# Kernel optimization log

Hardware: AMD Instinct MI355X
Metric: run time of the kernel (lower is better)

The kernel has to match this reference:

```python
import jax, jax.numpy as jnp
import numpy as np

B, C, H, W = 16, 256, 32, 32
AD, SC, R = 16, 32, 4


def _conv1x1(x, w, b):
    # x: [B,Cin,H,W], w: [Cout,Cin], b: [Cout]
    return jnp.einsum('oc,bchw->bohw', w, x) + b[None, :, None, None]


def setup_inputs() -> dict:
    key = jax.random.key(0)
    ks = jax.random.split(key, 12)
    p = lambda k, shape: (jax.random.normal(k, shape, dtype=jnp.float32) * 0.02)
    return {
        'x': jax.random.normal(ks[0], (B, C, H, W), dtype=jnp.float32),
        'fc1_w': p(ks[1], (C // R, C)), 'fc1_b': jnp.zeros((C // R,), jnp.float32),
        'fc2_w': p(ks[2], (C, C // R)), 'fc2_b': jnp.zeros((C,), jnp.float32),
        'qkv_w': p(ks[3], (AD * 2 + SC, SC)), 'qkv_b': jnp.zeros((AD * 2 + SC,), jnp.float32),
        'proj_w': p(ks[4], (SC, SC)), 'proj_b': jnp.zeros((SC,), jnp.float32),
        'ffn1_w': p(ks[5], (4 * C, C)), 'ffn1_b': jnp.zeros((4 * C,), jnp.float32),
        'ffn2_w': p(ks[6], (C, 4 * C)), 'ffn2_b': jnp.zeros((C,), jnp.float32),
    }


def reference(x, fc1_w, fc1_b, fc2_w, fc2_b, qkv_w, qkv_b, proj_w, proj_b,
              ffn1_w, ffn1_b, ffn2_w, ffn2_b):
    # --- DynamicChannelSelect: SE gate then channel split ---
    s = x.mean(axis=(2, 3), keepdims=True)                       # [B,C,1,1]
    s = jax.nn.relu(_conv1x1(s, fc1_w, fc1_b))
    s = jax.nn.sigmoid(_conv1x1(s, fc2_w, fc2_b))
    xg = x * s
    attn_part, non_attn_part = xg[:, :SC], xg[:, SC:]

    # --- SHSA: single-head self-attention on SC channels ---
    qkv = _conv1x1(attn_part, qkv_w, qkv_b)                      # [B,2*AD+SC,H,W]
    q = qkv[:, :AD].reshape(B, AD, H * W)
    k = qkv[:, AD:2 * AD].reshape(B, AD, H * W)
    v = qkv[:, 2 * AD:].reshape(B, SC, H * W)
    scale = AD ** -0.5
    attn = jax.nn.softmax(jnp.einsum('bcn,bcm->bnm', q, k) * scale, axis=-1)  # [B,N,N]
    out = jnp.einsum('bcm,bnm->bcn', v, attn).reshape(B, SC, H, W)
    attn_out = _conv1x1(out, proj_w, proj_b)

    # --- concat + 1x1-conv FFN ---
    y = jnp.concatenate([attn_out, non_attn_part], axis=1)       # [B,C,H,W]
    h = jax.nn.relu(_conv1x1(y, ffn1_w, ffn1_b))                 # [B,4C,H,W]
    return _conv1x1(h, ffn2_w, ffn2_b)                           # [B,C,H,W]
```

## Files before the change

kernel.cpp:

```cpp
#include <hip/hip_runtime.h>
#include <cstdint>
#include <cstddef>

#define BB 16
#define CC 256
#define NP 1024

typedef __attribute__((ext_vector_type(8))) short bf16x8;
typedef __attribute__((ext_vector_type(4))) float f32x4;
typedef unsigned short u16;

__device__ __forceinline__ u16 f2bf(float f) {
    union { float f; uint32_t u; } v; v.f = f;
    uint32_t u = v.u;
    return (u16)((u + 0x7FFFu + ((u >> 16) & 1u)) >> 16);
}

__global__ __launch_bounds__(256)
void se_mean_conv_kernel(const float* __restrict__ x, float* __restrict__ s_mean,
                         const float* __restrict__ w1, u16* __restrict__ d1,
                         const float* __restrict__ w2, u16* __restrict__ d2) {
    int blk = blockIdx.x;
    int t = threadIdx.x;
    if (blk < BB * CC) {
        const float* p = x + (size_t)blk * NP;
        float4 v = *(const float4*)(p + t * 4);
        float s = (v.x + v.y) + (v.z + v.w);
#pragma unroll
        for (int off = 32; off; off >>= 1) s += __shfl_down(s, off, 64);
        __shared__ float red[4];
        if ((t & 63) == 0) red[t >> 6] = s;
        __syncthreads();
        if (t == 0) s_mean[blk] = (red[0] + red[1] + red[2] + red[3]) * (1.0f / NP);
    } else {
        int blk2 = blk - BB * CC;
        const float* src = (blk2 < 256) ? w1 : w2;
        u16* dst = (blk2 < 256) ? d1 : d2;
        int i = ((blk2 & 255) * 256 + t) * 4;
        float4 v = *(const float4*)(src + i);
        ushort4 o;
        o.x = f2bf(v.x); o.y = f2bf(v.y); o.z = f2bf(v.z); o.w = f2bf(v.w);
        *(ushort4*)(dst + i) = o;
    }
}

__global__ __launch_bounds__(256)
void se_mlp_kernel(const float* __restrict__ s_mean,
                   const float* __restrict__ fc1_w, const float* __restrict__ fc1_b,
                   const float* __restrict__ fc2_w, const float* __restrict__ fc2_b,
                   float* __restrict__ sig) {
    int b = blockIdx.x, t = threadIdx.x;
    __shared__ float sm[256];
    __shared__ float part[4][64];
    __shared__ float h1[64];
    sm[t] = s_mean[b * 256 + t];
    __syncthreads();
    int to = t & 63, g = t >> 6;
    float a = 0.f;
#pragma unroll 8
    for (int c = 0; c < 64; ++c) a += fc1_w[to * 256 + g * 64 + c] * sm[g * 64 + c];
    part[g][to] = a;
    __syncthreads();
    if (t < 64) h1[t] = fmaxf(part[0][t] + part[1][t] + part[2][t] + part[3][t] + fc1_b[t], 0.f);
    __syncthreads();
    float acc = fc2_b[t];
#pragma unroll 8
    for (int j = 0; j < 64; ++j) acc += fc2_w[t * 64 + j] * h1[j];
    sig[b * 256 + t] = 1.f / (1.f + __expf(-acc));
}

__global__ __launch_bounds__(256)
void scale_transpose_qkv_kernel(const float* __restrict__ x, const float* __restrict__ sig,
                                const float* __restrict__ qW, const float* __restrict__ qB,
                                u16* __restrict__ ygt, u16* __restrict__ Qt,
                                u16* __restrict__ Kt, u16* __restrict__ Vb) {
    int nt = blockIdx.x, ct = blockIdx.y, b = blockIdx.z;
    __shared__ float tile[64][65];
    __shared__ float ws[64 * 32];
    __shared__ float bs[64];
    __shared__ float vtile[32][64];
    __shared__ float sig_l[64];
    int t = threadIdx.x;
    const float* Xb = x + ((size_t)b * CC + ct * 64) * NP + nt * 64;
    if (t < 64) sig_l[t] = sig[b * 256 + ct * 64 + t];
    if (ct == 0) {
        for (int e = t; e < 2048; e += 256) ws[e] = qW[e];
        if (t < 64) bs[t] = qB[t];
    }
#pragma unroll
    for (int p = 0; p < 4; ++p) {
        int e = t + p * 256;
        int c = e >> 4, n4 = (e & 15) * 4;
        float4 v = *(const float4*)&Xb[(size_t)c * NP + n4];
        tile[c][n4] = v.x; tile[c][n4 + 1] = v.y; tile[c][n4 + 2] = v.z; tile[c][n4 + 3] = v.w;
    }
    __syncthreads();
    u16* Yb = ygt + ((size_t)b * NP + nt * 64) * CC + ct * 64;
#pragma unroll
    for (int p = 0; p < 4; ++p) {
        int e = t + p * 256;
        int n = e >> 4, c4 = (e & 15) * 4;
        if (ct * 64 + c4 >= 32) {
            ushort4 o;
            o.x = f2bf(tile[c4][n] * sig_l[c4]);
            o.y = f2bf(tile[c4 + 1][n] * sig_l[c4 + 1]);
            o.z = f2bf(tile[c4 + 2][n] * sig_l[c4 + 2]);
            o.w = f2bf(tile[c4 + 3][n] * sig_l[c4 + 3]);
            *(ushort4*)&Yb[(size_t)n * CC + c4] = o;
        }
    }
    if (ct == 0) {
        int nn = t & 63, g = t >> 6;
        int n = nt * 64 + nn;
        float xs[32];
#pragma unroll
        for (int c = 0; c < 32; ++c) xs[c] = tile[c][nn] * sig_l[c];
        float acc[16];
#pragma unroll
        for (int oc = 0; oc < 16; ++oc) {
            int o = g * 16 + oc;
            float a = bs[o];
#pragma unroll
            for (int c = 0; c < 32; ++c) a += ws[o * 32 + c] * xs[c];
            acc[oc] = a;
        }
        if (g == 0) {
            u16* qr = Qt + ((size_t)b * NP + n) * 32;
            ushort4 z4; z4.x = 0; z4.y = 0; z4.z = 0; z4.w = 0;
#pragma unroll
            for (int j = 0; j < 16; j += 4) {
                ushort4 o4;
                o4.x = f2bf(acc[j] * 0.25f);     o4.y = f2bf(acc[j + 1] * 0.25f);
                o4.z = f2bf(acc[j + 2] * 0.25f); o4.w = f2bf(acc[j + 3] * 0.25f);
                *(ushort4*)&qr[j] = o4;
            }
            *(ushort4*)&qr[16] = z4; *(ushort4*)&qr[20] = z4;
            *(ushort4*)&qr[24] = z4; *(ushort4*)&qr[28] = z4;
        } else if (g == 1) {
            u16* kr = Kt + ((size_t)b * NP + n) * 32;
            ushort4 z4; z4.x = 0; z4.y = 0; z4.z = 0; z4.w = 0;
#pragma unroll
            for (int j = 0; j < 16; j += 4) {
                ushort4 k4;
                k4.x = f2bf(acc[j]);     k4.y = f2bf(acc[j + 1]);
                k4.z = f2bf(acc[j + 2]); k4.w = f2bf(acc[j + 3]);
                *(ushort4*)&kr[j] = k4;
            }
            *(ushort4*)&kr[16] = z4; *(ushort4*)&kr[20] = z4;
            *(ushort4*)&kr[24] = z4; *(ushort4*)&kr[28] = z4;
        } else {
#pragma unroll
            for (int oc = 0; oc < 16; ++oc) vtile[(g - 2) * 16 + oc][nn] = acc[oc];
        }
        __syncthreads();
        for (int e = t; e < 2048; e += 256) {
            int c = e >> 6, nn2 = e & 63;
            Vb[(size_t)b * 32 * NP + (size_t)c * NP + nt * 64 + nn2] = f2bf(vtile[c][nn2]);
        }
    }
}

__global__ __launch_bounds__(256)
void attn_mfma_kernel(const u16* __restrict__ Qt, const u16* __restrict__ Kt,
                      const u16* __restrict__ Vb,
                      const float* __restrict__ proj_w, const float* __restrict__ proj_b,
                      u16* __restrict__ ygt) {
    int b = blockIdx.x & 15;
    int n0 = (blockIdx.x >> 4) * 16;
    __shared__ __align__(16) u16 P_lds[4][16][40];
    __shared__ float al_lds[4][16];
    __shared__ float sm_lds[4][16];
    __shared__ float sl_lds[4][16];
    __shared__ float O_lds[4][16][33];
    __shared__ float pw_s[32][32];
    __shared__ float pb_s[32];
    int t = threadIdx.x;
    int w = t >> 6, lane = t & 63;
    int q = lane >> 4, idx = lane & 15;

    for (int e = t; e < 1024; e += 256) pw_s[e >> 5][e & 31] = proj_w[e];
    if (t < 32) pb_s[t] = proj_b[t];
    __syncthreads();

    const u16* Qb = Qt + (size_t)b * NP * 32;
    const u16* Kb = Kt + (size_t)b * NP * 32;
    const u16* Vp = Vb + (size_t)b * 32 * NP;

    int nrow = n0 + idx;
    bf16x8 aq = *(const bf16x8*)&Qb[(size_t)nrow * 32 + q * 8];

    f32x4 O0 = {0.f, 0.f, 0.f, 0.f}, O1 = {0.f, 0.f, 0.f, 0.f};
    float m_run[4] = {-1e30f, -1e30f, -1e30f, -1e30f};
    float l_run[4] = {0.f, 0.f, 0.f, 0.f};

    int mbase = w * 256;
    for (int m0 = mbase; m0 < mbase + 256; m0 += 32) {
        bf16x8 bk0 = *(const bf16x8*)&Kb[(size_t)(m0 + idx) * 32 + q * 8];
        bf16x8 bk1 = *(const bf16x8*)&Kb[(size_t)(m0 + 16 + idx) * 32 + q * 8];
        bf16x8 va0 = *(const bf16x8*)&Vp[(size_t)idx * NP + m0 + q * 8];
        bf16x8 va1 = *(const bf16x8*)&Vp[(size_t)(16 + idx) * NP + m0 + q * 8];
        f32x4 z = {0.f, 0.f, 0.f, 0.f};
        f32x4 S0 = __builtin_amdgcn_mfma_f32_16x16x32_bf16(aq, bk0, z, 0, 0, 0);
        f32x4 S1 = __builtin_amdgcn_mfma_f32_16x16x32_bf16(aq, bk1, z, 0, 0, 0);
        float mx[4], p0[4], p1[4], alpha[4];
#pragma unroll
        for (int r = 0; r < 4; ++r) mx[r] = fmaxf(S0[r], S1[r]);
#pragma unroll
        for (int off = 1; off < 16; off <<= 1)
#pragma unroll
            for (int r = 0; r < 4; ++r) mx[r] = fmaxf(mx[r], __shfl_xor(mx[r], off, 64));
#pragma unroll
        for (int r = 0; r < 4; ++r) {
            float nm = fmaxf(m_run[r], mx[r]);
            alpha[r] = __expf(m_run[r] - nm);
            m_run[r] = nm;
            p0[r] = __expf(S0[r] - nm);
            p1[r] = __expf(S1[r] - nm);
        }
#pragma unroll
        for (int r = 0; r < 4; ++r) {
            float s = p0[r] + p1[r];
#pragma unroll
            for (int off = 1; off < 16; off <<= 1) s += __shfl_xor(s, off, 64);
            l_run[r] = l_run[r] * alpha[r] + s;
        }
#pragma unroll
        for (int r = 0; r < 4; ++r) {
            P_lds[w][q * 4 + r][idx]      = f2bf(p0[r]);
            P_lds[w][q * 4 + r][idx + 16] = f2bf(p1[r]);
        }
        if (idx == 0) {
#pragma unroll
            for (int r = 0; r < 4; ++r) al_lds[w][q * 4 + r] = alpha[r];
        }
        float an = al_lds[w][idx];
#pragma unroll
        for (int r = 0; r < 4; ++r) { O0[r] *= an; O1[r] *= an; }
        bf16x8 pf = *(const bf16x8*)&P_lds[w][idx][q * 8];
        O0 = __builtin_amdgcn_mfma_f32_16x16x32_bf16(va0, pf, O0, 0, 0, 0);
        O1 = __builtin_amdgcn_mfma_f32_16x16x32_bf16(va1, pf, O1, 0, 0, 0);
    }
    if (idx == 0) {
#pragma unroll
        for (int r = 0; r < 4; ++r) {
            sm_lds[w][q * 4 + r] = m_run[r];
            sl_lds[w][q * 4 + r] = l_run[r];
        }
    }
#pragma unroll
    for (int r = 0; r < 4; ++r) {
        O_lds[w][idx][q * 4 + r]      = O0[r];
        O_lds[w][idx][q * 4 + r + 16] = O1[r];
    }
    __syncthreads();
    if (w == 0) {
        float m0_ = sm_lds[0][idx], m1 = sm_lds[1][idx], m2 = sm_lds[2][idx], m3 = sm_lds[3][idx];
        float gm = fmaxf(fmaxf(m0_, m1), fmaxf(m2, m3));
        float e0 = __expf(m0_ - gm), e1 = __expf(m1 - gm);
        float e2 = __expf(m2 - gm), e3 = __expf(m3 - gm);
        float linv = 1.f / (sl_lds[0][idx] * e0 + sl_lds[1][idx] * e1 +
                            sl_lds[2][idx] * e2 + sl_lds[3][idx] * e3);
#pragma unroll
        for (int r = 0; r < 4; ++r) {
            int c0 = q * 4 + r;
            O_lds[0][idx][c0] = (O_lds[0][idx][c0] * e0 + O_lds[1][idx][c0] * e1 +
                                 O_lds[2][idx][c0] * e2 + O_lds[3][idx][c0] * e3) * linv;
            int c1 = c0 + 16;
            O_lds[0][idx][c1] = (O_lds[0][idx][c1] * e0 + O_lds[1][idx][c1] * e1 +
                                 O_lds[2][idx][c1] * e2 + O_lds[3][idx][c1] * e3) * linv;
        }
        float o0[4], o1[4];
#pragma unroll
        for (int r = 0; r < 4; ++r) { o0[r] = pb_s[q * 4 + r]; o1[r] = pb_s[q * 4 + r + 16]; }
#pragma unroll
        for (int c = 0; c < 32; ++c) {
            float xv = O_lds[0][idx][c];
#pragma unroll
            for (int r = 0; r < 4; ++r) {
                o0[r] += pw_s[q * 4 + r][c] * xv;
                o1[r] += pw_s[q * 4 + r + 16][c] * xv;
            }
        }
        u16* yrow = ygt + ((size_t)b * NP + n0 + idx) * CC;
        ushort4 w0, w1;
        w0.x = f2bf(o0[0]); w0.y = f2bf(o0[1]); w0.z = f2bf(o0[2]); w0.w = f2bf(o0[3]);
        w1.x = f2bf(o1[0]); w1.y = f2bf(o1[1]); w1.z = f2bf(o1[2]); w1.w = f2bf(o1[3]);
        *(ushort4*)&yrow[q * 4] = w0;
        *(ushort4*)&yrow[q * 4 + 16] = w1;
    }
}

__global__ __launch_bounds__(512, 2)
void ffn_fused_kernel(const u16* __restrict__ w1b, const u16* __restrict__ w2b,
                      const u16* __restrict__ ygt,
                      const float* __restrict__ bias1, const float* __restrict__ bias2,
                      float* __restrict__ out) {
    __shared__ __align__(16) u16 Ys[4][64][64];
    __shared__ __align__(16) u16 Hs[2][64][64];
    __shared__ __align__(16) u16 W2s[2][256][64];
    __shared__ float Bs1[1024];
    int t = threadIdx.x;
    int w = t >> 6, lane = t & 63;
    int q = lane >> 4, idx = lane & 15;
    int srow = lane >> 3;
    int gch = (lane & 7) ^ srow;
    int n0 = blockIdx.x * 64;
    int rot = blockIdx.x & 7;
    int hh = w >> 2, wm = w & 3;

#define ISSUE_W2S(sc_)                                                                     \
    {                                                                                      \
        _Pragma("unroll")                                                                  \
        for (int e = 0; e < 8; ++e) {                                                      \
            int hh2 = e >> 2, rnd = e & 3;                                                 \
            int rw = rnd * 64 + w * 8;                                                     \
            __builtin_amdgcn_global_load_lds(                                              \
                (const __attribute__((address_space(1))) void*)(w2b + (size_t)(rw + srow) * 1024 + (sc_) * 128 + hh2 * 64 + gch * 8), \
                (__attribute__((address_space(3))) void*)(&W2s[hh2][rw][0]),               \
                16, 0, 0);                                                                 \
        }                                                                                  \
    }

#define LOAD_AF(dst, sc_)                                                                  \
    {                                                                                      \
        const u16* a1 = w1b + ((size_t)((sc_) * 128 + w * 16 + idx)) * CC;                 \
        _Pragma("unroll")                                                                  \
        for (int s = 0; s < 8; ++s) dst[s] = *(const bf16x8*)(a1 + s * 32 + q * 8);        \
    }

#pragma unroll
    for (int e = 0; e < 4; ++e) {
        __builtin_amdgcn_global_load_lds(
            (const __attribute__((address_space(1))) void*)(ygt + (size_t)(n0 + w * 8 + srow) * CC + e * 64 + gch * 8),
            (__attribute__((address_space(3))) void*)(&Ys[e][w * 8][0]),
            16, 0, 0);
    }
    Bs1[t] = bias1[t];
    Bs1[t + 512] = bias1[t + 512];

    f32x4 oacc[4][4];
#pragma unroll
    for (int f = 0; f < 4; ++f)
#pragma unroll
        for (int j = 0; j < 4; ++j) { f32x4 z = {0.f, 0.f, 0.f, 0.f}; oacc[f][j] = z; }

    ISSUE_W2S(rot)
    bf16x8 af[8];
    LOAD_AF(af, rot)
    __syncthreads();

    for (int it = 0; it < 8; ++it) {
        int sc  = (it + rot) & 7;
        int scn = (it + 1 + rot) & 7;
        bf16x8 afn[8];
        if (it + 1 < 8) LOAD_AF(afn, scn)

        f32x4 hacc[4];
#pragma unroll
        for (int j = 0; j < 4; ++j) { f32x4 z = {0.f, 0.f, 0.f, 0.f}; hacc[j] = z; }
#pragma unroll
        for (int s = 0; s < 8; ++s) {
            int kb = s >> 1, h2 = s & 1;
#pragma unroll
            for (int j = 0; j < 4; ++j) {
                bf16x8 yb = *(const bf16x8*)&Ys[kb][j * 16 + idx][(((q + 4 * h2) ^ (idx & 7)) * 8)];
                hacc[j] = __builtin_amdgcn_mfma_f32_16x16x32_bf16(af[s], yb, hacc[j], 0, 0, 0);
            }
        }

        int mb = sc * 128 + w * 16 + q * 4;
        float b0 = Bs1[mb], b1v = Bs1[mb + 1], b2v = Bs1[mb + 2], b3v = Bs1[mb + 3];
        int chk_hi = wm * 2 + (q >> 1);
#pragma unroll
        for (int j = 0; j < 4; ++j) {
            int n = j * 16 + idx;
            int chk = chk_hi ^ (n & 7);
            uint32_t lo = (uint32_t)f2bf(fmaxf(hacc[j][0] + b0, 0.f)) |
                          ((uint32_t)f2bf(fmaxf(hacc[j][1] + b1v, 0.f)) << 16);
            uint32_t hi = (uint32_t)f2bf(fmaxf(hacc[j][2] + b2v, 0.f)) |
                          ((uint32_t)f2bf(fmaxf(hacc[j][3] + b3v, 0.f)) << 16);
            uint32_t* hp = (uint32_t*)&Hs[hh][n][chk * 8 + (q & 1) * 4];
            hp[0] = lo; hp[1] = hi;
        }
        __syncthreads();

#pragma unroll
        for (int s2 = 0; s2 < 2; ++s2) {
            bf16x8 a2f[4];
#pragma unroll
            for (int f = 0; f < 4; ++f)
                a2f[f] = *(const bf16x8*)&W2s[hh][wm * 64 + f * 16 + idx][(((q + 4 * s2) ^ (idx & 7)) * 8)];
#pragma unroll
            for (int j = 0; j < 4; ++j) {
                bf16x8 hb = *(const bf16x8*)&Hs[hh][j * 16 + idx][(((q + 4 * s2) ^ (idx & 7)) * 8)];
#pragma unroll
                for (int f = 0; f < 4; ++f)
                    oacc[f][j] = __builtin_amdgcn_mfma_f32_16x16x32_bf16(a2f[f], hb, oacc[f][j], 0, 0, 0);
            }
        }
        __syncthreads();

        if (it + 1 < 8) {
            ISSUE_W2S(scn)
#pragma unroll
            for (int s = 0; s < 8; ++s) af[s] = afn[s];
        }
    }
#undef ISSUE_W2S
#undef LOAD_AF

    float* R = (float*)&W2s[0][0][0];
    if (w >= 4) {
#pragma unroll
        for (int f = 0; f < 4; ++f)
#pragma unroll
            for (int j = 0; j < 4; ++j)
#pragma unroll
                for (int r = 0; r < 4; ++r)
                    R[(wm * 64 + f * 16 + q * 4 + r) * 64 + j * 16 + idx] = oacc[f][j][r];
    }
    __syncthreads();
    if (w < 4) {
        int b = n0 >> 10, nnb = n0 & 1023;
#pragma unroll
        for (int f = 0; f < 4; ++f) {
            int m2 = wm * 64 + f * 16 + q * 4;
            float c0 = bias2[m2], c1 = bias2[m2 + 1], c2 = bias2[m2 + 2], c3 = bias2[m2 + 3];
#pragma unroll
            for (int j = 0; j < 4; ++j) {
                int col = j * 16 + idx;
                const float* Rp = &R[m2 * 64 + col];
                float* p = out + ((size_t)b * CC + m2) * NP + nnb + col;
                f32x4 v = oacc[f][j];
                p[0]      = v.x + c0 + Rp[0];
                p[NP]     = v.y + c1 + Rp[64];
                p[2 * NP] = v.z + c2 + Rp[128];
                p[3 * NP] = v.w + c3 + Rp[192];
            }
        }
    }
}

extern "C" void kernel_launch(void* const* d_in, const int* in_sizes, int n_in,
                              void* d_out, int out_size, void* d_ws, size_t ws_size,
                              hipStream_t stream) {
    const float* x      = (const float*)d_in[0];
    const float* fc1_w  = (const float*)d_in[1];
    const float* fc1_b  = (const float*)d_in[2];
    const float* fc2_w  = (const float*)d_in[3];
    const float* fc2_b  = (const float*)d_in[4];
    const float* qkv_w  = (const float*)d_in[5];
    const float* qkv_b  = (const float*)d_in[6];
    const float* proj_w = (const float*)d_in[7];
    const float* proj_b = (const float*)d_in[8];
    const float* ffn1_w = (const float*)d_in[9];
    const float* ffn1_b = (const float*)d_in[10];
    const float* ffn2_w = (const float*)d_in[11];
    const float* ffn2_b = (const float*)d_in[12];
    float* out = (float*)d_out;

    u16* w1b = (u16*)d_ws;
    u16* w2b = w1b + 262144;
    u16* ygt = w2b + 262144;
    u16* scratch = ygt + (size_t)BB * NP * CC;
    float* s_mean = (float*)scratch;
    float* sig    = s_mean + BB * CC;
    u16* Qt = (u16*)(sig + BB * CC);
    u16* Kt = Qt + (size_t)BB * NP * 32;
    u16* Vb = Kt + (size_t)BB * NP * 32;

    se_mean_conv_kernel<<<BB * CC + 512, 256, 0, stream>>>(x, s_mean, ffn1_w, w1b, ffn2_w, w2b);
    se_mlp_kernel<<<BB, 256, 0, stream>>>(s_mean, fc1_w, fc1_b, fc2_w, fc2_b, sig);
    scale_transpose_qkv_kernel<<<dim3(16, 4, BB), 256, 0, stream>>>(
        x, sig, qkv_w, qkv_b, ygt, Qt, Kt, Vb);
    attn_mfma_kernel<<<BB * 64, 256, 0, stream>>>(Qt, Kt, Vb, proj_w, proj_b, ygt);

    ffn_fused_kernel<<<256, 512, 0, stream>>>(w1b, w2b, ygt, ffn1_b, ffn2_b, out);
}
```

Baseline: 162.7 us.

## Restructure fused FFN into 4 wide hidden chunks with double-buffered W2 pipeline

Reworks the fused FFN kernel so each of the 8 waves computes 32 hidden rows per step (256 hidden per step, 4 steps instead of 8), and in the second GEMM each wave owns 32 output channels over the full hidden slice. The cross-wave split of the second GEMM and the final LDS reduction are removed. W2 tiles are streamed in 64-wide chunks into a double buffer with explicit vmcnt waits and raw barriers to overlap loads with MFMA work. This increases register pressure (two A-fragment sets and hidden accumulators) and adds more barriers per step. The manual waitcnt counts must match the outstanding loads exactly to stay correct.

```diff
diff --git a/kernel.cpp b/kernel.cpp
--- a/kernel.cpp
+++ b/kernel.cpp
@@ -296,7 +296,7 @@
                       const float* __restrict__ bias1, const float* __restrict__ bias2,
                       float* __restrict__ out) {
     __shared__ __align__(16) u16 Ys[4][64][64];
-    __shared__ __align__(16) u16 Hs[2][64][64];
+    __shared__ __align__(16) u16 Hs[64][256];
     __shared__ __align__(16) u16 W2s[2][256][64];
     __shared__ float Bs1[1024];
     int t = threadIdx.x;
@@ -305,28 +305,36 @@
     int srow = lane >> 3;
     int gch = (lane & 7) ^ srow;
     int n0 = blockIdx.x * 64;
-    int rot = blockIdx.x & 7;
-    int hh = w >> 2, wm = w & 3;
-
-#define ISSUE_W2S(sc_)                                                                     \
-    {                                                                                      \
-        _Pragma("unroll")                                                                  \
-        for (int e = 0; e < 8; ++e) {                                                      \
-            int hh2 = e >> 2, rnd = e & 3;                                                 \
-            int rw = rnd * 64 + w * 8;                                                     \
-            __builtin_amdgcn_global_load_lds(                                              \
-                (const __attribute__((address_space(1))) void*)(w2b + (size_t)(rw + srow) * 1024 + (sc_) * 128 + hh2 * 64 + gch * 8), \
-                (__attribute__((address_space(3))) void*)(&W2s[hh2][rw][0]),               \
-                16, 0, 0);                                                                 \
-        }                                                                                  \
-    }
-
-#define LOAD_AF(dst, sc_)                                                                  \
-    {                                                                                      \
-        const u16* a1 = w1b + ((size_t)((sc_) * 128 + w * 16 + idx)) * CC;                 \
-        _Pragma("unroll")                                                                  \
-        for (int s = 0; s < 8; ++s) dst[s] = *(const bf16x8*)(a1 + s * 32 + q * 8);        \
-    }
+    int rot = blockIdx.x & 3;
+
+#define BAR_SYNC { __builtin_amdgcn_s_barrier(); __builtin_amdgcn_sched_barrier(0); }
+
+#define ISSUE_CHUNK(gp_, buf_)                                                            \
+    {                                                                                     \
+        _Pragma("unroll")                                                                 \
+        for (int e = 0; e < 4; ++e) {                                                     \
+            __builtin_amdgcn_global_load_lds(                                             \
+                (const __attribute__((address_space(1))) void*)(w2b + (size_t)(e * 64 + w * 8 + srow) * 1024 + (gp_) * 64 + gch * 8), \
+                (__attribute__((address_space(3))) void*)(&W2s[buf_][e * 64 + w * 8][0]), \
+                16, 0, 0);                                                                \
+        }                                                                                 \
+    }
+
+#define LOAD_AF(scp_)                                                                     \
+    {                                                                                     \
+        const u16* a1 = w1b + ((size_t)((scp_) * 256 + w * 32 + idx)) * CC;               \
+        _Pragma("unroll")                                                                 \
+        for (int i2 = 0; i2 < 2; ++i2)                                                    \
+            _Pragma("unroll")                                                             \
+            for (int s = 0; s < 8; ++s)                                                   \
+                af[i2][s] = *(const bf16x8*)(a1 + i2 * 16 * CC + s * 32 + q * 8);         \
+    }
+
+    Bs1[t] = bias1[t];
+    Bs1[t + 512] = bias1[t + 512];
+
+    bf16x8 af[2][8];
+    LOAD_AF(rot)
 
 #pragma unroll
     for (int e = 0; e < 4; ++e) {
@@ -335,108 +343,118 @@
             (__attribute__((address_space(3))) void*)(&Ys[e][w * 8][0]),
             16, 0, 0);
     }
-    Bs1[t] = bias1[t];
-    Bs1[t + 512] = bias1[t + 512];
-
-    f32x4 oacc[4][4];
-#pragma unroll
-    for (int f = 0; f < 4; ++f)
-#pragma unroll
-        for (int j = 0; j < 4; ++j) { f32x4 z = {0.f, 0.f, 0.f, 0.f}; oacc[f][j] = z; }
-
-    ISSUE_W2S(rot)
-    bf16x8 af[8];
-    LOAD_AF(af, rot)
-    __syncthreads();
-
-    for (int it = 0; it < 8; ++it) {
-        int sc  = (it + rot) & 7;
-        int scn = (it + 1 + rot) & 7;
-        bf16x8 afn[8];
-        if (it + 1 < 8) LOAD_AF(afn, scn)
-
-        f32x4 hacc[4];
-#pragma unroll
-        for (int j = 0; j < 4; ++j) { f32x4 z = {0.f, 0.f, 0.f, 0.f}; hacc[j] = z; }
+    ISSUE_CHUNK(rot * 4 + 0, 0)
+    ISSUE_CHUNK(rot * 4 + 1, 1)
+
+    f32x4 oacc[2][4];
+#pragma unroll
+    for (int i2 = 0; i2 < 2; ++i2)
+#pragma unroll
+        for (int j = 0; j < 4; ++j) { f32x4 z = {0.f, 0.f, 0.f, 0.f}; oacc[i2][j] = z; }
+
+    asm volatile("s_waitcnt vmcnt(8) lgkmcnt(0)" ::: "memory");
+    BAR_SYNC
+
+    for (int sc = 0; sc < 4; ++sc) {
+        int scp = (sc + rot) & 3;
+
+        f32x4 hacc[2][4];
+#pragma unroll
+        for (int i2 = 0; i2 < 2; ++i2)
+#pragma unroll
+            for (int j = 0; j < 4; ++j) { f32x4 z = {0.f, 0.f, 0.f, 0.f}; hacc[i2][j] = z; }
 #pragma unroll
         for (int s = 0; s < 8; ++s) {
             int kb = s >> 1, h2 = s & 1;
 #pragma unroll
             for (int j = 0; j < 4; ++j) {
                 bf16x8 yb = *(const bf16x8*)&Ys[kb][j * 16 + idx][(((q + 4 * h2) ^ (idx & 7)) * 8)];
-                hacc[j] = __builtin_amdgcn_mfma_f32_16x16x32_bf16(af[s], yb, hacc[j], 0, 0, 0);
-            }
-        }
-
-        int mb = sc * 128 + w * 16 + q * 4;
-        float b0 = Bs1[mb], b1v = Bs1[mb + 1], b2v = Bs1[mb + 2], b3v = Bs1[mb + 3];
-        int chk_hi = wm * 2 + (q >> 1);
+                hacc[0][j] = __builtin_amdgcn_mfma_f32_16x16x32_bf16(af[0][s], yb, hacc[0][j], 0, 0, 0);
+                hacc[1][j] = __builtin_amdgcn_mfma_f32_16x16x32_bf16(af[1][s], yb, hacc[1][j], 0, 0, 0);
+            }
+        }
+
+        asm volatile("s_waitcnt lgkmcnt(0)" ::: "memory");
+        BAR_SYNC
+
+#pragma unroll
+        for (int i2 = 0; i2 < 2; ++i2) {
+            int cc2 = (2 * w + i2) >> 2;
+            int g8 = ((2 * w + i2) & 3) * 2 + (q >> 1);
+            int mb = scp * 256 + w * 32 + i2 * 16 + q * 4;
+            float b0 = Bs1[mb & 1023], b1v = Bs1[(mb + 1) & 1023];
+            float b2v = Bs1[(mb + 2) & 1023], b3v = Bs1[(mb + 3) & 1023];
+#pragma unroll
+            for (int j = 0; j < 4; ++j) {
+                int n = j * 16 + idx;
+                uint32_t lo = (uint32_t)f2bf(fmaxf(hacc[i2][j][0] + b0, 0.f)) |
+                              ((uint32_t)f2bf(fmaxf(hacc[i2][j][1] + b1v, 0.f)) << 16);
+                uint32_t hi = (uint32_t)f2bf(fmaxf(hacc[i2][j][2] + b2v, 0.f)) |
+                              ((uint32_t)f2bf(fmaxf(hacc[i2][j][3] + b3v, 0.f)) << 16);
+                uint32_t* hp = (uint32_t*)&Hs[n][cc2 * 64 + ((g8 ^ (n & 7)) * 8) + (q & 1) * 4];
+                hp[0] = lo; hp[1] = hi;
+            }
+        }
+
+#pragma unroll
+        for (int c = 0; c < 4; ++c) {
+            if (c == 3) {
+                if (sc == 3) { asm volatile("s_waitcnt vmcnt(0)"  ::: "memory"); }
+                else         { asm volatile("s_waitcnt vmcnt(20)" ::: "memory"); }
+            } else {
+                asm volatile("s_waitcnt vmcnt(4)" ::: "memory");
+            }
+            asm volatile("s_waitcnt lgkmcnt(0)" ::: "memory");
+            BAR_SYNC
+
+            const u16 (*W2r)[64] = W2s[c & 1];
+#pragma unroll
+            for (int s2 = 0; s2 < 2; ++s2) {
+                bf16x8 a2f[2], hb[4];
+#pragma unroll
+                for (int i2 = 0; i2 < 2; ++i2)
+                    a2f[i2] = *(const bf16x8*)&W2r[w * 32 + i2 * 16 + idx][(((q + 4 * s2) ^ (idx & 7)) * 8)];
+#pragma unroll
+                for (int j = 0; j < 4; ++j)
+                    hb[j] = *(const bf16x8*)&Hs[j * 16 + idx][c * 64 + (((q + 4 * s2) ^ (idx & 7)) * 8)];
+#pragma unroll
+                for (int i2 = 0; i2 < 2; ++i2)
+#pragma unroll
+                    for (int j = 0; j < 4; ++j)
+                        oacc[i2][j] = __builtin_amdgcn_mfma_f32_16x16x32_bf16(a2f[i2], hb[j], oacc[i2][j], 0, 0, 0);
+            }
+
+            asm volatile("s_waitcnt lgkmcnt(0)" ::: "memory");
+            BAR_SYNC
+
+            if (c == 2 && sc < 3) LOAD_AF((scp + 1) & 3)
+            {
+                int l = sc * 4 + c;
+                if (l + 2 < 16) {
+                    int lp = l + 2;
+                    int gp = ((((lp >> 2) + rot) & 3) << 2) | (lp & 3);
+                    ISSUE_CHUNK(gp, (c & 1))
+                }
+            }
+        }
+    }
+#undef ISSUE_CHUNK
+#undef LOAD_AF
+#undef BAR_SYNC
+
+    int b = n0 >> 10, nnb = n0 & 1023;
+#pragma unroll
+    for (int i2 = 0; i2 < 2; ++i2) {
+        int m2 = w * 32 + i2 * 16 + q * 4;
+        float4 bv = *(const float4*)&bias2[m2];
 #pragma unroll
         for (int j = 0; j < 4; ++j) {
-            int n = j * 16 + idx;
-            int chk = chk_hi ^ (n & 7);
-            uint32_t lo = (uint32_t)f2bf(fmaxf(hacc[j][0] + b0, 0.f)) |
-                          ((uint32_t)f2bf(fmaxf(hacc[j][1] + b1v, 0.f)) << 16);
-            uint32_t hi = (uint32_t)f2bf(fmaxf(hacc[j][2] + b2v, 0.f)) |
-                          ((uint32_t)f2bf(fmaxf(hacc[j][3] + b3v, 0.f)) << 16);
-            uint32_t* hp = (uint32_t*)&Hs[hh][n][chk * 8 + (q & 1) * 4];
-            hp[0] = lo; hp[1] = hi;
-        }
-        __syncthreads();
-
-#pragma unroll
-        for (int s2 = 0; s2 < 2; ++s2) {
-            bf16x8 a2f[4];
-#pragma unroll
-            for (int f = 0; f < 4; ++f)
-                a2f[f] = *(const bf16x8*)&W2s[hh][wm * 64 + f * 16 + idx][(((q + 4 * s2) ^ (idx & 7)) * 8)];
-#pragma unroll
-            for (int j = 0; j < 4; ++j) {
-                bf16x8 hb = *(const bf16x8*)&Hs[hh][j * 16 + idx][(((q + 4 * s2) ^ (idx & 7)) * 8)];
-#pragma unroll
-                for (int f = 0; f < 4; ++f)
-                    oacc[f][j] = __builtin_amdgcn_mfma_f32_16x16x32_bf16(a2f[f], hb, oacc[f][j], 0, 0, 0);
-            }
-        }
-        __syncthreads();
-
-        if (it + 1 < 8) {
-            ISSUE_W2S(scn)
-#pragma unroll
-            for (int s = 0; s < 8; ++s) af[s] = afn[s];
-        }
-    }
-#undef ISSUE_W2S
-#undef LOAD_AF
-
-    float* R = (float*)&W2s[0][0][0];
-    if (w >= 4) {
-#pragma unroll
-        for (int f = 0; f < 4; ++f)
-#pragma unroll
-            for (int j = 0; j < 4; ++j)
-#pragma unroll
-                for (int r = 0; r < 4; ++r)
-                    R[(wm * 64 + f * 16 + q * 4 + r) * 64 + j * 16 + idx] = oacc[f][j][r];
-    }
-    __syncthreads();
-    if (w < 4) {
-        int b = n0 >> 10, nnb = n0 & 1023;
-#pragma unroll
-        for (int f = 0; f < 4; ++f) {
-            int m2 = wm * 64 + f * 16 + q * 4;
-            float c0 = bias2[m2], c1 = bias2[m2 + 1], c2 = bias2[m2 + 2], c3 = bias2[m2 + 3];
-#pragma unroll
-            for (int j = 0; j < 4; ++j) {
-                int col = j * 16 + idx;
-                const float* Rp = &R[m2 * 64 + col];
-                float* p = out + ((size_t)b * CC + m2) * NP + nnb + col;
-                f32x4 v = oacc[f][j];
-                p[0]      = v.x + c0 + Rp[0];
-                p[NP]     = v.y + c1 + Rp[64];
-                p[2 * NP] = v.z + c2 + Rp[128];
-                p[3 * NP] = v.w + c3 + Rp[192];
-            }
+            float* p = out + ((size_t)b * CC + m2) * NP + nnb + j * 16 + idx;
+            f32x4 v = oacc[i2][j];
+            p[0]      = v.x + bv.x;
+            p[NP]     = v.y + bv.y;
+            p[2 * NP] = v.z + bv.z;
+            p[3 * NP] = v.w + bv.w;
         }
     }
 }
```

Result: slower. 170.0 us (+4.5%).
